# Kernel optimization log

Measured on AMD Instinct MI355X. Metric: run time of the kernel, lower is better.

The kernel has to match this reference:

```python
import jax, jax.numpy as jnp
import numpy as np

TEMP = 0.07
BASE_TEMP = 0.07
EPS = 1e-12


def setup_inputs() -> dict:
    key = jax.random.key(0)
    k1, k2, k3 = jax.random.split(key, 3)
    B, V, D, C = 4096, 1, 128, 100
    features = jax.random.normal(k1, (B, V, D), dtype=jnp.float32)
    labels = jax.random.randint(k2, (B,), 0, C, dtype=jnp.int64)
    covariances = jax.random.normal(k3, (C, D, D), dtype=jnp.float32)
    return {"features": features, "labels": labels, "covariances": covariances}


def reference(features, labels, covariances):
    B, n_views = features.shape[0], features.shape[1]
    feats = features.reshape(B, n_views, -1)
    # cat(unbind(dim=1), dim=0); with n_views==1 this is feats[:, 0]
    contrast_feature = jnp.concatenate([feats[:, v] for v in range(n_views)], axis=0)
    anchor_feature = contrast_feature  # contrast_mode == 'all'

    # mask_{i,j} = 1 if labels match
    mask = (labels[:, None] == labels[None, :]).astype(jnp.float32)  # [B,B]

    similarity_matrix = anchor_feature @ contrast_feature.T  # [B,B]

    # dis[i,j] = a_i^T C_{label_i} a_j  (gather cov per anchor, one bilinear form per pair)
    cov_g = covariances[labels]                              # [B,D,D] irregular gather
    v = jnp.einsum('id,ide->ie', anchor_feature, cov_g)      # [B,D]
    dis_matrix = v @ anchor_feature.T                        # [B,B]

    logits = (similarity_matrix + dis_matrix / (2.0 * TEMP ** 2)) / TEMP
    logits = logits - jax.lax.stop_gradient(jnp.max(logits, axis=1, keepdims=True))
    log_prob = logits - jnp.log(jnp.sum(jnp.exp(logits), axis=1, keepdims=True) + EPS)

    # original: (mask[:,:,None] * log_prob).sum(1) == mask @ log_prob (avoids B^3 temp)
    mask_sum = mask.sum(axis=1, keepdims=True)               # [B,1]
    mean_log_prob_pos = (mask @ log_prob) / (mask_sum + EPS)  # [B,B]
    loss = -(TEMP / BASE_TEMP) * mean_log_prob_pos
    return loss.mean()
```

## Files before the change

### kernel.cpp

```cpp
#include <hip/hip_runtime.h>
#include <hip/hip_bf16.h>


#define DIM 128
#define TEMP 0.07f

typedef __attribute__((ext_vector_type(8))) short short8;
typedef __attribute__((ext_vector_type(4))) float floatx4;

static __device__ __forceinline__ unsigned short f2bf(float f) {
    __hip_bfloat16 h = __float2bfloat16(f);
    union { __hip_bfloat16 h; unsigned short u; } c;
    c.h = h;
    return c.u;
}

__global__ __launch_bounds__(256) void prep_kernel(
    const float* __restrict__ A, const int* __restrict__ labels,
    const float* __restrict__ Cov, unsigned short* __restrict__ Wbf,
    unsigned short* __restrict__ Abf) {
    const float inv2t2 = 1.0f / (2.0f * TEMP * TEMP);
    const float invt = 1.0f / TEMP;
    const int sub = threadIdx.x >> 7;
    const int e = threadIdx.x & 127;
    const int i = blockIdx.x * 2 + sub;
    __shared__ float a[2][DIM];
    float av = A[(size_t)i * DIM + e];
    a[sub][e] = av;
    Abf[(size_t)i * DIM + e] = f2bf(av);
    __syncthreads();
    int c = labels[i];
    const float* Cp = Cov + (size_t)c * (DIM * DIM) + e;
    float acc = 0.0f;
#pragma unroll 8
    for (int d = 0; d < DIM; ++d) {
        acc = fmaf(a[sub][d], Cp[(size_t)d * DIM], acc);
    }
    Wbf[(size_t)i * DIM + e] = f2bf((av + acc * inv2t2) * invt);
}

__global__ __launch_bounds__(256, 2) void main_kernel(
    const unsigned short* __restrict__ Wbf, const unsigned short* __restrict__ Abf,
    float* __restrict__ mP, float* __restrict__ zP, float* __restrict__ sP,
    int Jsplit, int JSWEEP, int nP) {
    __shared__ __align__(16) unsigned short sW[128 * 128];
    __shared__ __align__(16) unsigned short sA[64 * 128];

    const int mb = blockIdx.x / Jsplit;
    const int jsp = blockIdx.x % Jsplit;
    const int rowBase = mb * 128;
    const int t = threadIdx.x;
    const int wave = t >> 6, lane = t & 63, quad = lane >> 4, l16 = lane & 15;
    const int waveM = wave >> 1, waveN = wave & 1;

    {
        int row = t >> 1, half = t & 1, rsw = row & 15;
        const unsigned short* src = Wbf + (size_t)(rowBase + row) * DIM + half * 64;
        unsigned short* dstrow = sW + row * 128;
#pragma unroll
        for (int i = 0; i < 8; i++) {
            int c = half * 8 + i;
            *(short8*)(dstrow + ((c ^ rsw) << 3)) = *(const short8*)(src + i * 8);
        }
    }

    float run_m[4][4], run_Z[4][4], run_s[4][4];
#pragma unroll
    for (int a = 0; a < 4; a++)
#pragma unroll
        for (int r = 0; r < 4; r++) {
            run_m[a][r] = -3.4e38f; run_Z[a][r] = 0.f; run_s[a][r] = 0.f;
        }

    const int arow = t >> 2, aq = t & 3, arsw = arow & 15;
    const unsigned short* asrc0 =
        Abf + (size_t)(jsp * JSWEEP * 64 + arow) * DIM + aq * 32;
    unsigned short* adst = sA + arow * 128;

    short8 pre[4];
#pragma unroll
    for (int i = 0; i < 4; i++) pre[i] = *(const short8*)(asrc0 + i * 8);

    const unsigned short* myW = sW + (size_t)(waveM * 64 + l16) * 128;
    const unsigned short* myA = sA + (size_t)(waveN * 32 + l16) * 128;

    for (int js = 0; js < JSWEEP; ++js) {
        __syncthreads();
#pragma unroll
        for (int i = 0; i < 4; i++) {
            int c = aq * 4 + i;
            *(short8*)(adst + ((c ^ arsw) << 3)) = pre[i];
        }
        __syncthreads();

        if (js + 1 < JSWEEP) {
            const unsigned short* nsrc = asrc0 + (size_t)(js + 1) * 64 * DIM;
#pragma unroll
            for (int i = 0; i < 4; i++) pre[i] = *(const short8*)(nsrc + i * 8);
        }

        floatx4 acc[4][2];
#pragma unroll
        for (int mt = 0; mt < 4; mt++)
#pragma unroll
            for (int nt = 0; nt < 2; nt++) acc[mt][nt] = (floatx4)0.f;

#pragma unroll
        for (int kst = 0; kst < 4; ++kst) {
            const int coff = (((kst << 2) | quad) ^ l16) << 3;
            short8 bfrag[2];
#pragma unroll
            for (int nt = 0; nt < 2; nt++)
                bfrag[nt] = *(const short8*)(myA + nt * 16 * 128 + coff);
#pragma unroll
            for (int mt = 0; mt < 4; mt++) {
                short8 afrag = *(const short8*)(myW + mt * 16 * 128 + coff);
#pragma unroll
                for (int nt = 0; nt < 2; nt++)
                    acc[mt][nt] = __builtin_amdgcn_mfma_f32_16x16x32_bf16(
                        afrag, bfrag[nt], acc[mt][nt], 0, 0, 0);
            }
        }

#pragma unroll
        for (int mt = 0; mt < 4; mt++)
#pragma unroll
            for (int r = 0; r < 4; r++) {
                float v0 = acc[mt][0][r], v1 = acc[mt][1][r];
                float tm = fmaxf(v0, v1);
                float nm = fmaxf(run_m[mt][r], tm);
                run_Z[mt][r] = run_Z[mt][r] * __expf(run_m[mt][r] - nm)
                             + __expf(v0 - nm) + __expf(v1 - nm);
                run_m[mt][r] = nm;
                run_s[mt][r] += v0 + v1;
            }
    }

    const int chunk = jsp * 2 + waveN;
#pragma unroll
    for (int mt = 0; mt < 4; mt++)
#pragma unroll
        for (int r = 0; r < 4; r++) {
            float m = run_m[mt][r], Z = run_Z[mt][r], s = run_s[mt][r];
#pragma unroll
            for (int mask = 1; mask < 16; mask <<= 1) {
                float om = __shfl_xor(m, mask);
                float oZ = __shfl_xor(Z, mask);
                float os = __shfl_xor(s, mask);
                float nm = fmaxf(m, om);
                Z = Z * __expf(m - nm) + oZ * __expf(om - nm);
                m = nm;
                s += os;
            }
            if (l16 == r) {
                int row = rowBase + waveM * 64 + mt * 16 + quad * 4 + r;
                size_t idx = (size_t)row * nP + chunk;
                mP[idx] = m; zP[idx] = Z; sP[idx] = s;
            }
        }
}

__global__ __launch_bounds__(64) void combine_kernel(
    const float* __restrict__ mP, const float* __restrict__ zP,
    const float* __restrict__ sP, double* __restrict__ Sk, int B, int nP) {
    int k = blockIdx.x;
    int l = threadIdx.x;
    float m = -3.4e38f, Z = 0.0f, s = 0.0f;
    if (l < nP) {
        size_t idx = (size_t)k * nP + l;
        m = mP[idx]; Z = zP[idx]; s = sP[idx];
    }
    float M = m;
#pragma unroll
    for (int o = 32; o > 0; o >>= 1) M = fmaxf(M, __shfl_xor(M, o));
    float zt = Z * __expf(m - M);
    float st = s;
#pragma unroll
    for (int o = 32; o > 0; o >>= 1) {
        zt += __shfl_xor(zt, o);
        st += __shfl_xor(st, o);
    }
    if (l == 0) {
        Sk[k] = (double)st - (double)B * (double)M
                - (double)B * log((double)zt + 1e-12);
    }
}

__global__ __launch_bounds__(1024) void final_kernel(
    const double* __restrict__ Sk, const int* __restrict__ labels,
    float* __restrict__ out, int B) {
    __shared__ int hist[128];
    __shared__ double sh[1024];
    int t = threadIdx.x;
    if (t < 128) hist[t] = 0;
    __syncthreads();
    for (int i = t; i < B; i += 1024) atomicAdd(&hist[labels[i]], 1);
    __syncthreads();
    double acc = 0.0;
    for (int i = t; i < B; i += 1024) {
        double cnt = (double)hist[labels[i]];
        acc += Sk[i] * (cnt / (cnt + 1e-12));
    }
    sh[t] = acc;
    __syncthreads();
    for (int o = 512; o > 0; o >>= 1) {
        if (t < o) sh[t] += sh[t + o];
        __syncthreads();
    }
    if (t == 0) out[0] = (float)(-sh[0] / ((double)B * (double)B));
}

extern "C" void kernel_launch(void* const* d_in, const int* in_sizes, int n_in,
                              void* d_out, int out_size, void* d_ws, size_t ws_size,
                              hipStream_t stream) {
    const float* A = (const float*)d_in[0];
    const int* labels = (const int*)d_in[1];
    const float* Cov = (const float*)d_in[2];
    float* out = (float*)d_out;

    int B = in_sizes[0] / DIM;
    int Jsplit = 16;
    int JSWEEP = B / (Jsplit * 64);
    int nP = Jsplit * 2;

    char* ws = (char*)d_ws;
    unsigned short* Wbf = (unsigned short*)ws;
    unsigned short* Abf = Wbf + (size_t)B * DIM;
    float* mP = (float*)(Abf + (size_t)B * DIM);
    float* zP = mP + (size_t)B * nP;
    float* sP = zP + (size_t)B * nP;
    double* Sk = (double*)(sP + (size_t)B * nP);

    prep_kernel<<<B / 2, 256, 0, stream>>>(A, labels, Cov, Wbf, Abf);
    main_kernel<<<(B / 128) * Jsplit, 256, 0, stream>>>(Wbf, Abf, mP, zP, sP,
                                                        Jsplit, JSWEEP, nP);
    combine_kernel<<<B, 64, 0, stream>>>(mP, zP, sP, Sk, B, nP);
    final_kernel<<<1, 1024, 0, stream>>>(Sk, labels, out, B);
}
```

Baseline: 101.0 us.

## Convert covariances to bf16, vectorize prep, fuse combine and final via ticket

Adds a pass that converts the covariance tensor to bf16 so the gathered bilinear prep reads half the bytes, and vectorizes prep to handle 4 outputs per thread with 8 rows per block. Partial softmax stats are stored chunk-major so a new tail kernel can combine them with coalesced loads. That tail kernel also does the final reduction in its last block, chosen with an atomic ticket, which replaces two launches with one. This adds an extra conversion launch over 100x128x128 elements and lowers the precision of the covariance product to bf16.

```diff
diff --git a/kernel.cpp b/kernel.cpp
--- a/kernel.cpp
+++ b/kernel.cpp
@@ -15,34 +15,68 @@
     return c.u;
 }
 
+static __device__ __forceinline__ float bf2f(unsigned short u) {
+    union { unsigned int u; float f; } c;
+    c.u = ((unsigned int)u) << 16;
+    return c.f;
+}
+
+__global__ __launch_bounds__(256) void conv_kernel(
+    const float* __restrict__ Cov, unsigned short* __restrict__ Covbf,
+    int* __restrict__ ticket, int n) {
+    int i = (blockIdx.x * 256 + threadIdx.x) * 4;
+    if (i == 0) *ticket = 0;
+    if (i < n) {
+        float4 v = *(const float4*)(Cov + i);
+        ushort4 o;
+        o.x = f2bf(v.x); o.y = f2bf(v.y); o.z = f2bf(v.z); o.w = f2bf(v.w);
+        *(ushort4*)(Covbf + i) = o;
+    }
+}
+
 __global__ __launch_bounds__(256) void prep_kernel(
     const float* __restrict__ A, const int* __restrict__ labels,
-    const float* __restrict__ Cov, unsigned short* __restrict__ Wbf,
+    const unsigned short* __restrict__ Covbf, unsigned short* __restrict__ Wbf,
     unsigned short* __restrict__ Abf) {
     const float inv2t2 = 1.0f / (2.0f * TEMP * TEMP);
     const float invt = 1.0f / TEMP;
-    const int sub = threadIdx.x >> 7;
-    const int e = threadIdx.x & 127;
-    const int i = blockIdx.x * 2 + sub;
-    __shared__ float a[2][DIM];
-    float av = A[(size_t)i * DIM + e];
-    a[sub][e] = av;
-    Abf[(size_t)i * DIM + e] = f2bf(av);
+    const int t = threadIdx.x;
+    const int sub = t >> 5, q = t & 31;
+    const int i = blockIdx.x * 8 + sub;
+    __shared__ float a[8][DIM];
+    float4 av = *(const float4*)(A + (size_t)i * DIM + 4 * q);
+    a[sub][4 * q + 0] = av.x;
+    a[sub][4 * q + 1] = av.y;
+    a[sub][4 * q + 2] = av.z;
+    a[sub][4 * q + 3] = av.w;
+    ushort4 ab;
+    ab.x = f2bf(av.x); ab.y = f2bf(av.y); ab.z = f2bf(av.z); ab.w = f2bf(av.w);
+    *(ushort4*)(Abf + (size_t)i * DIM + 4 * q) = ab;
     __syncthreads();
     int c = labels[i];
-    const float* Cp = Cov + (size_t)c * (DIM * DIM) + e;
-    float acc = 0.0f;
+    const unsigned short* Cp = Covbf + (size_t)c * (DIM * DIM) + 4 * q;
+    float4 acc = make_float4(0.f, 0.f, 0.f, 0.f);
 #pragma unroll 8
     for (int d = 0; d < DIM; ++d) {
-        acc = fmaf(a[sub][d], Cp[(size_t)d * DIM], acc);
-    }
-    Wbf[(size_t)i * DIM + e] = f2bf((av + acc * inv2t2) * invt);
+        ushort4 cv = *(const ushort4*)(Cp + (size_t)d * DIM);
+        float ad = a[sub][d];
+        acc.x = fmaf(ad, bf2f(cv.x), acc.x);
+        acc.y = fmaf(ad, bf2f(cv.y), acc.y);
+        acc.z = fmaf(ad, bf2f(cv.z), acc.z);
+        acc.w = fmaf(ad, bf2f(cv.w), acc.w);
+    }
+    ushort4 w;
+    w.x = f2bf((av.x + acc.x * inv2t2) * invt);
+    w.y = f2bf((av.y + acc.y * inv2t2) * invt);
+    w.z = f2bf((av.z + acc.z * inv2t2) * invt);
+    w.w = f2bf((av.w + acc.w * inv2t2) * invt);
+    *(ushort4*)(Wbf + (size_t)i * DIM + 4 * q) = w;
 }
 
 __global__ __launch_bounds__(256, 2) void main_kernel(
     const unsigned short* __restrict__ Wbf, const unsigned short* __restrict__ Abf,
     float* __restrict__ mP, float* __restrict__ zP, float* __restrict__ sP,
-    int Jsplit, int JSWEEP, int nP) {
+    int Jsplit, int JSWEEP, int nP, int B) {
     __shared__ __align__(16) unsigned short sW[128 * 128];
     __shared__ __align__(16) unsigned short sA[64 * 128];
 
@@ -154,56 +188,54 @@
             }
             if (l16 == r) {
                 int row = rowBase + waveM * 64 + mt * 16 + quad * 4 + r;
-                size_t idx = (size_t)row * nP + chunk;
+                size_t idx = (size_t)chunk * B + row;
                 mP[idx] = m; zP[idx] = Z; sP[idx] = s;
             }
         }
 }
 
-__global__ __launch_bounds__(64) void combine_kernel(
+__global__ __launch_bounds__(256) void tail_kernel(
     const float* __restrict__ mP, const float* __restrict__ zP,
-    const float* __restrict__ sP, double* __restrict__ Sk, int B, int nP) {
-    int k = blockIdx.x;
-    int l = threadIdx.x;
-    float m = -3.4e38f, Z = 0.0f, s = 0.0f;
-    if (l < nP) {
-        size_t idx = (size_t)k * nP + l;
-        m = mP[idx]; Z = zP[idx]; s = sP[idx];
-    }
-    float M = m;
-#pragma unroll
-    for (int o = 32; o > 0; o >>= 1) M = fmaxf(M, __shfl_xor(M, o));
-    float zt = Z * __expf(m - M);
-    float st = s;
-#pragma unroll
-    for (int o = 32; o > 0; o >>= 1) {
-        zt += __shfl_xor(zt, o);
-        st += __shfl_xor(st, o);
-    }
-    if (l == 0) {
-        Sk[k] = (double)st - (double)B * (double)M
-                - (double)B * log((double)zt + 1e-12);
-    }
-}
-
-__global__ __launch_bounds__(1024) void final_kernel(
-    const double* __restrict__ Sk, const int* __restrict__ labels,
-    float* __restrict__ out, int B) {
+    const float* __restrict__ sP, const int* __restrict__ labels,
+    double* __restrict__ Sk, int* __restrict__ ticket,
+    float* __restrict__ out, int B, int nP) {
+    __shared__ int flag;
     __shared__ int hist[128];
-    __shared__ double sh[1024];
-    int t = threadIdx.x;
+    __shared__ double sh[256];
+    const int t = threadIdx.x;
+    const int k = blockIdx.x * 256 + t;
+
+    float m = mP[k], Z = zP[k], s = sP[k];
+    for (int p = 1; p < nP; ++p) {
+        size_t idx = (size_t)p * B + k;
+        float mi = mP[idx];
+        float nm = fmaxf(m, mi);
+        Z = Z * __expf(m - nm) + zP[idx] * __expf(mi - nm);
+        m = nm;
+        s += sP[idx];
+    }
+    Sk[k] = (double)s - (double)B * (double)m
+            - (double)B * log((double)Z + 1e-12);
+
+    __threadfence();
+    __syncthreads();
+    if (t == 0) flag = (atomicAdd(ticket, 1) == (int)gridDim.x - 1);
+    __syncthreads();
+    if (!flag) return;
+    __threadfence();
+
     if (t < 128) hist[t] = 0;
     __syncthreads();
-    for (int i = t; i < B; i += 1024) atomicAdd(&hist[labels[i]], 1);
+    for (int i = t; i < B; i += 256) atomicAdd(&hist[labels[i]], 1);
     __syncthreads();
     double acc = 0.0;
-    for (int i = t; i < B; i += 1024) {
+    for (int i = t; i < B; i += 256) {
         double cnt = (double)hist[labels[i]];
         acc += Sk[i] * (cnt / (cnt + 1e-12));
     }
     sh[t] = acc;
     __syncthreads();
-    for (int o = 512; o > 0; o >>= 1) {
+    for (int o = 128; o > 0; o >>= 1) {
         if (t < o) sh[t] += sh[t + o];
         __syncthreads();
     }
@@ -219,21 +251,26 @@
     float* out = (float*)d_out;
 
     int B = in_sizes[0] / DIM;
+    int nCov = in_sizes[2];
     int Jsplit = 16;
     int JSWEEP = B / (Jsplit * 64);
     int nP = Jsplit * 2;
 
     char* ws = (char*)d_ws;
-    unsigned short* Wbf = (unsigned short*)ws;
+    unsigned short* Covbf = (unsigned short*)ws;
+    unsigned short* Wbf = Covbf + (size_t)nCov;
     unsigned short* Abf = Wbf + (size_t)B * DIM;
     float* mP = (float*)(Abf + (size_t)B * DIM);
     float* zP = mP + (size_t)B * nP;
     float* sP = zP + (size_t)B * nP;
     double* Sk = (double*)(sP + (size_t)B * nP);
-
-    prep_kernel<<<B / 2, 256, 0, stream>>>(A, labels, Cov, Wbf, Abf);
+    int* ticket = (int*)(Sk + B);
+
+    conv_kernel<<<(nCov / 4 + 255) / 256, 256, 0, stream>>>(Cov, Covbf,
+                                                            ticket, nCov);
+    prep_kernel<<<B / 8, 256, 0, stream>>>(A, labels, Covbf, Wbf, Abf);
     main_kernel<<<(B / 128) * Jsplit, 256, 0, stream>>>(Wbf, Abf, mP, zP, sP,
-                                                        Jsplit, JSWEEP, nP);
-    combine_kernel<<<B, 64, 0, stream>>>(mP, zP, sP, Sk, B, nP);
-    final_kernel<<<1, 1024, 0, stream>>>(Sk, labels, out, B);
-}
+                                                        Jsplit, JSWEEP, nP, B);
+    tail_kernel<<<B / 256, 256, 0, stream>>>(mP, zP, sP, labels, Sk, ticket,
+                                             out, B, nP);
+}
```

Result: slower. 112.5 us (+11.3%).
